# Performance work log

Hardware: AMD Instinct MI355X
Metric: run time of the kernel (lower is better)

The kernel has to match this reference:

```python
import jax, jax.numpy as jnp
import numpy as np

N, NQ, M, DQ, DK, DV, H = 4, 512, 512, 256, 256, 256, 256


def setup_inputs() -> dict:
    key = jax.random.key(0)
    ks = jax.random.split(key, 6)
    scale_q = 1.0 / np.sqrt(DQ)
    scale_k = 1.0 / np.sqrt(DK)
    scale_v = 1.0 / np.sqrt(H)
    return {
        "query": jax.random.normal(ks[0], (N, NQ, DQ), jnp.float32),
        "key": jax.random.normal(ks[1], (N, M, DK), jnp.float32),
        "value": jax.random.normal(ks[2], (N, M, DV), jnp.float32),
        "W_q": jax.random.normal(ks[3], (DQ, H), jnp.float32) * scale_q,
        "W_k": jax.random.normal(ks[4], (DK, H), jnp.float32) * scale_k,
        "W_v": jax.random.normal(ks[5], (H,), jnp.float32) * scale_v,
    }


def reference(query, key, value, W_q, W_k, W_v):
    # project: (N, n, H) and (N, m, H)
    q = jnp.einsum("bnd,dh->bnh", query, W_q)
    k = jnp.einsum("bmd,dh->bmh", key, W_k)
    # broadcast add -> (N, n, m, H), tanh, project H->1 -> scores (N, n, m)
    scores = jnp.einsum("bnmh,h->bnm", jnp.tanh(q[:, :, None, :] + k[:, None, :, :]), W_v)
    attn = jax.nn.softmax(scores, axis=-1)  # (N, n, m)
    return jnp.einsum("bnm,bmv->bnv", attn, value)
```

## Files before the change

kernel.cpp:

```cpp
#include <hip/hip_runtime.h>
#include <hip/hip_bf16.h>

#define NB 4
#define NQL 512
#define ML 512
#define DDIM 256
#define HDIM 256

static constexpr float TWO_LOG2E = 2.8853900817779268f;
static constexpr float LOG2E     = 1.4426950408889634f;

__global__ __launch_bounds__(256) void proj_kernel(
    const float* __restrict__ q_src, const float* __restrict__ k_src,
    const float* __restrict__ Wq,    const float* __restrict__ Wk,
    float* __restrict__ EqT,         float* __restrict__ EkT)
{
    const int z = blockIdx.z;
    const int b = z & 3;
    const int which = z >> 2;
    const float* __restrict__ src  = which ? k_src : q_src;
    const float* __restrict__ W    = which ? Wk    : Wq;
    float* __restrict__       outT = which ? EkT   : EqT;

    const int l0 = blockIdx.x * 32;
    const int h0 = blockIdx.y * 64;
    const int t  = threadIdx.x;
    const int tx = t & 15;
    const int ty = t >> 4;

    __shared__ float sX[32][36];
    __shared__ float sW[32][68];

    float acc[2][4];
    #pragma unroll
    for (int i = 0; i < 2; i++)
        #pragma unroll
        for (int j = 0; j < 4; j++) acc[i][j] = 0.f;

    const int llA = t >> 3, dgA = t & 7;
    const int ddB = t >> 3, hgB = t & 7;

    for (int d0 = 0; d0 < DDIM; d0 += 32) {
        float4 xv = *(const float4*)&src[(size_t)(b * NQL + l0 + llA) * DDIM + d0 + dgA * 4];
        const float* wrow = &W[(size_t)(d0 + ddB) * HDIM + h0 + hgB * 8];
        float4 wa = ((const float4*)wrow)[0];
        float4 wb = ((const float4*)wrow)[1];
        __syncthreads();
        sX[dgA * 4 + 0][llA] = xv.x;
        sX[dgA * 4 + 1][llA] = xv.y;
        sX[dgA * 4 + 2][llA] = xv.z;
        sX[dgA * 4 + 3][llA] = xv.w;
        *(float4*)&sW[ddB][hgB * 8]     = wa;
        *(float4*)&sW[ddB][hgB * 8 + 4] = wb;
        __syncthreads();
        #pragma unroll
        for (int dd = 0; dd < 32; dd++) {
            float4 w4 = *(const float4*)&sW[dd][tx * 4];
            float2 x2 = *(const float2*)&sX[dd][ty * 2];
            acc[0][0] = fmaf(x2.x, w4.x, acc[0][0]);
            acc[0][1] = fmaf(x2.x, w4.y, acc[0][1]);
            acc[0][2] = fmaf(x2.x, w4.z, acc[0][2]);
            acc[0][3] = fmaf(x2.x, w4.w, acc[0][3]);
            acc[1][0] = fmaf(x2.y, w4.x, acc[1][0]);
            acc[1][1] = fmaf(x2.y, w4.y, acc[1][1]);
            acc[1][2] = fmaf(x2.y, w4.z, acc[1][2]);
            acc[1][3] = fmaf(x2.y, w4.w, acc[1][3]);
        }
    }

    #pragma unroll
    for (int j = 0; j < 4; j++) {
        float2 o;
        o.x = __builtin_amdgcn_exp2f(acc[0][j] * TWO_LOG2E);
        o.y = __builtin_amdgcn_exp2f(acc[1][j] * TWO_LOG2E);
        *(float2*)&outT[(size_t)(b * HDIM + h0 + tx * 4 + j) * NQL + l0 + ty * 2] = o;
    }
}

__global__ __launch_bounds__(256) void scores_kernel(
    const float* __restrict__ EqT, const float* __restrict__ EkT,
    const float* __restrict__ Wv, float* __restrict__ S)
{
    const int b  = blockIdx.z;
    const int m0 = blockIdx.x * 32;
    const int n0 = blockIdx.y * 32;
    const int t  = threadIdx.x;
    const int tx = t & 15;
    const int ty = t >> 4;

    __shared__ float sQ[32][36];
    __shared__ float sK[32][36];
    __shared__ float sWV[32];

    float acc00 = 0.f, acc01 = 0.f, acc10 = 0.f, acc11 = 0.f;
    float swv = 0.f;

    const int hhA = t >> 3, cgA = t & 7;

    for (int h0 = 0; h0 < HDIM; h0 += 32) {
        float4 qv = *(const float4*)&EqT[(size_t)(b * HDIM + h0 + hhA) * NQL + n0 + cgA * 4];
        float4 kv = *(const float4*)&EkT[(size_t)(b * HDIM + h0 + hhA) * ML  + m0 + cgA * 4];
        float wv_ld = (t < 32) ? Wv[h0 + t] : 0.f;
        __syncthreads();
        *(float4*)&sQ[hhA][cgA * 4] = qv;
        *(float4*)&sK[hhA][cgA * 4] = kv;
        if (t < 32) sWV[t] = wv_ld;
        __syncthreads();
        #pragma unroll 8
        for (int hh = 0; hh < 32; hh++) {
            float2 q2 = *(const float2*)&sQ[hh][ty * 2];
            float2 k2 = *(const float2*)&sK[hh][tx * 2];
            float wv = sWV[hh];
            swv += wv;
            const float nw2 = -2.0f * wv;
            float a00 = fmaf(q2.x, k2.x, 1.0f);
            float a01 = fmaf(q2.x, k2.y, 1.0f);
            float a10 = fmaf(q2.y, k2.x, 1.0f);
            float a11 = fmaf(q2.y, k2.y, 1.0f);
            float r0 = __builtin_amdgcn_rcpf(a00 * a01);
            float r1 = __builtin_amdgcn_rcpf(a10 * a11);
            acc00 = fmaf(nw2, r0 * a01, acc00);
            acc01 = fmaf(nw2, r0 * a00, acc01);
            acc10 = fmaf(nw2, r1 * a11, acc10);
            acc11 = fmaf(nw2, r1 * a10, acc11);
        }
    }

    float2 o0 = {swv + acc00, swv + acc01};
    float2 o1 = {swv + acc10, swv + acc11};
    *(float2*)&S[(size_t)(b * NQL + n0 + ty * 2 + 0) * ML + m0 + tx * 2] = o0;
    *(float2*)&S[(size_t)(b * NQL + n0 + ty * 2 + 1) * ML + m0 + tx * 2] = o1;
}

__global__ __launch_bounds__(256) void softmax_kernel(float* __restrict__ S)
{
    const int row = blockIdx.x;
    float* p = &S[(size_t)row * ML];
    const int t = threadIdx.x;
    const int lane = t & 63, wid = t >> 6;

    float a = p[t];
    float c = p[t + 256];
    float mx = fmaxf(a, c);
    #pragma unroll
    for (int off = 32; off > 0; off >>= 1)
        mx = fmaxf(mx, __shfl_down(mx, off, 64));

    __shared__ float red[8];
    if (lane == 0) red[wid] = mx;
    __syncthreads();
    mx = fmaxf(fmaxf(red[0], red[1]), fmaxf(red[2], red[3]));

    float e0 = __builtin_amdgcn_exp2f((a - mx) * LOG2E);
    float e1 = __builtin_amdgcn_exp2f((c - mx) * LOG2E);
    float s = e0 + e1;
    #pragma unroll
    for (int off = 32; off > 0; off >>= 1)
        s += __shfl_down(s, off, 64);
    if (lane == 0) red[4 + wid] = s;
    __syncthreads();
    const float tot = red[4] + red[5] + red[6] + red[7];
    const float inv = 1.0f / tot;
    p[t]       = e0 * inv;
    p[t + 256] = e1 * inv;
}

__global__ __launch_bounds__(256) void av_kernel(
    const float* __restrict__ A, const float* __restrict__ V,
    float* __restrict__ O)
{
    const int b  = blockIdx.z;
    const int v0 = blockIdx.x * 64;
    const int n0 = blockIdx.y * 16;
    const int t  = threadIdx.x;
    const int tx = t & 15;
    const int ty = t >> 4;

    __shared__ float sA[32][20];
    __shared__ float sV[32][68];

    float4 acc = {0.f, 0.f, 0.f, 0.f};

    const int nnA = t >> 4, mgA = t & 15;
    const int mmB = t >> 3, vgB = t & 7;

    for (int m0 = 0; m0 < ML; m0 += 32) {
        float2 av = *(const float2*)&A[(size_t)(b * NQL + n0 + nnA) * ML + m0 + mgA * 2];
        const float* vrow = &V[(size_t)(b * ML + m0 + mmB) * DDIM + v0 + vgB * 8];
        float4 va = ((const float4*)vrow)[0];
        float4 vb = ((const float4*)vrow)[1];
        __syncthreads();
        sA[mgA * 2 + 0][nnA] = av.x;
        sA[mgA * 2 + 1][nnA] = av.y;
        *(float4*)&sV[mmB][vgB * 8]     = va;
        *(float4*)&sV[mmB][vgB * 8 + 4] = vb;
        __syncthreads();
        #pragma unroll
        for (int mm = 0; mm < 32; mm++) {
            float a = sA[mm][ty];
            float4 v4 = *(const float4*)&sV[mm][tx * 4];
            acc.x = fmaf(a, v4.x, acc.x);
            acc.y = fmaf(a, v4.y, acc.y);
            acc.z = fmaf(a, v4.z, acc.z);
            acc.w = fmaf(a, v4.w, acc.w);
        }
    }

    *(float4*)&O[(size_t)(b * NQL + n0 + ty) * DDIM + v0 + tx * 4] = acc;
}

extern "C" void kernel_launch(void* const* d_in, const int* in_sizes, int n_in,
                              void* d_out, int out_size, void* d_ws, size_t ws_size,
                              hipStream_t stream)
{
    const float* query = (const float*)d_in[0];
    const float* key   = (const float*)d_in[1];
    const float* value = (const float*)d_in[2];
    const float* Wq    = (const float*)d_in[3];
    const float* Wk    = (const float*)d_in[4];
    const float* Wv    = (const float*)d_in[5];
    float* out = (float*)d_out;

    float* EqT = (float*)d_ws;
    float* EkT = EqT + (size_t)NB * HDIM * NQL;
    float* S   = EkT + (size_t)NB * HDIM * ML;

    dim3 gProj(NQL / 32, HDIM / 64, NB * 2);
    proj_kernel<<<gProj, 256, 0, stream>>>(query, key, Wq, Wk, EqT, EkT);

    dim3 gSc(ML / 32, NQL / 32, NB);
    scores_kernel<<<gSc, 256, 0, stream>>>(EqT, EkT, Wv, S);

    softmax_kernel<<<dim3(NB * NQL), 256, 0, stream>>>(S);

    dim3 gAv(DDIM / 64, NQL / 16, NB);
    av_kernel<<<gAv, 256, 0, stream>>>(S, value, out);
}
```

Before: 133.7 us.

## Fuse softmax into scores and AV kernels via partial row sums

Drops the standalone softmax kernel. The scores kernel now writes unnormalized exponentials of the scores and per-tile partial row sums. The AV kernel sums these partials and scales its output by the reciprocal. This removes a kernel launch and a full read/write pass over the score matrix. It relies on scores being bounded, since no row max is subtracted, so it carries overflow risk for large weights.

```diff
diff --git a/kernel.cpp b/kernel.cpp
--- a/kernel.cpp
+++ b/kernel.cpp
@@ -79,10 +79,12 @@
 
 __global__ __launch_bounds__(256) void scores_kernel(
     const float* __restrict__ EqT, const float* __restrict__ EkT,
-    const float* __restrict__ Wv, float* __restrict__ S)
+    const float* __restrict__ Wv, float* __restrict__ P,
+    float* __restrict__ Spart)
 {
     const int b  = blockIdx.z;
-    const int m0 = blockIdx.x * 32;
+    const int mt = blockIdx.x;
+    const int m0 = mt * 32;
     const int n0 = blockIdx.y * 32;
     const int t  = threadIdx.x;
     const int tx = t & 15;
@@ -126,48 +128,30 @@
         }
     }
 
-    float2 o0 = {swv + acc00, swv + acc01};
-    float2 o1 = {swv + acc10, swv + acc11};
-    *(float2*)&S[(size_t)(b * NQL + n0 + ty * 2 + 0) * ML + m0 + tx * 2] = o0;
-    *(float2*)&S[(size_t)(b * NQL + n0 + ty * 2 + 1) * ML + m0 + tx * 2] = o1;
-}
-
-__global__ __launch_bounds__(256) void softmax_kernel(float* __restrict__ S)
-{
-    const int row = blockIdx.x;
-    float* p = &S[(size_t)row * ML];
-    const int t = threadIdx.x;
-    const int lane = t & 63, wid = t >> 6;
-
-    float a = p[t];
-    float c = p[t + 256];
-    float mx = fmaxf(a, c);
+    float2 o0, o1;
+    o0.x = __builtin_amdgcn_exp2f((swv + acc00) * LOG2E);
+    o0.y = __builtin_amdgcn_exp2f((swv + acc01) * LOG2E);
+    o1.x = __builtin_amdgcn_exp2f((swv + acc10) * LOG2E);
+    o1.y = __builtin_amdgcn_exp2f((swv + acc11) * LOG2E);
+    *(float2*)&P[(size_t)(b * NQL + n0 + ty * 2 + 0) * ML + m0 + tx * 2] = o0;
+    *(float2*)&P[(size_t)(b * NQL + n0 + ty * 2 + 1) * ML + m0 + tx * 2] = o1;
+
+    float rs0 = o0.x + o0.y;
+    float rs1 = o1.x + o1.y;
     #pragma unroll
-    for (int off = 32; off > 0; off >>= 1)
-        mx = fmaxf(mx, __shfl_down(mx, off, 64));
-
-    __shared__ float red[8];
-    if (lane == 0) red[wid] = mx;
-    __syncthreads();
-    mx = fmaxf(fmaxf(red[0], red[1]), fmaxf(red[2], red[3]));
-
-    float e0 = __builtin_amdgcn_exp2f((a - mx) * LOG2E);
-    float e1 = __builtin_amdgcn_exp2f((c - mx) * LOG2E);
-    float s = e0 + e1;
-    #pragma unroll
-    for (int off = 32; off > 0; off >>= 1)
-        s += __shfl_down(s, off, 64);
-    if (lane == 0) red[4 + wid] = s;
-    __syncthreads();
-    const float tot = red[4] + red[5] + red[6] + red[7];
-    const float inv = 1.0f / tot;
-    p[t]       = e0 * inv;
-    p[t + 256] = e1 * inv;
+    for (int off = 1; off < 16; off <<= 1) {
+        rs0 += __shfl_xor(rs0, off);
+        rs1 += __shfl_xor(rs1, off);
+    }
+    if (tx == 0) {
+        Spart[(size_t)(mt * NB + b) * NQL + n0 + ty * 2 + 0] = rs0;
+        Spart[(size_t)(mt * NB + b) * NQL + n0 + ty * 2 + 1] = rs1;
+    }
 }
 
 __global__ __launch_bounds__(256) void av_kernel(
-    const float* __restrict__ A, const float* __restrict__ V,
-    float* __restrict__ O)
+    const float* __restrict__ A, const float* __restrict__ Spart,
+    const float* __restrict__ V, float* __restrict__ O)
 {
     const int b  = blockIdx.z;
     const int v0 = blockIdx.x * 64;
@@ -178,6 +162,15 @@
 
     __shared__ float sA[32][20];
     __shared__ float sV[32][68];
+    __shared__ float sInv[16];
+
+    if (t < 16) {
+        float s = 0.f;
+        #pragma unroll
+        for (int mt = 0; mt < 16; ++mt)
+            s += Spart[(size_t)(mt * NB + b) * NQL + n0 + t];
+        sInv[t] = 1.0f / s;
+    }
 
     float4 acc = {0.f, 0.f, 0.f, 0.f};
 
@@ -206,7 +199,13 @@
         }
     }
 
-    *(float4*)&O[(size_t)(b * NQL + n0 + ty) * DDIM + v0 + tx * 4] = acc;
+    const float inv = sInv[ty];
+    float4 o;
+    o.x = acc.x * inv;
+    o.y = acc.y * inv;
+    o.z = acc.z * inv;
+    o.w = acc.w * inv;
+    *(float4*)&O[(size_t)(b * NQL + n0 + ty) * DDIM + v0 + tx * 4] = o;
 }
 
 extern "C" void kernel_launch(void* const* d_in, const int* in_sizes, int n_in,
@@ -221,18 +220,17 @@
     const float* Wv    = (const float*)d_in[5];
     float* out = (float*)d_out;
 
-    float* EqT = (float*)d_ws;
-    float* EkT = EqT + (size_t)NB * HDIM * NQL;
-    float* S   = EkT + (size_t)NB * HDIM * ML;
+    float* EqT   = (float*)d_ws;
+    float* EkT   = EqT + (size_t)NB * HDIM * NQL;
+    float* P     = EkT + (size_t)NB * HDIM * ML;
+    float* Spart = P + (size_t)NB * NQL * ML;
 
     dim3 gProj(NQL / 32, HDIM / 64, NB * 2);
     proj_kernel<<<gProj, 256, 0, stream>>>(query, key, Wq, Wk, EqT, EkT);
 
     dim3 gSc(ML / 32, NQL / 32, NB);
-    scores_kernel<<<gSc, 256, 0, stream>>>(EqT, EkT, Wv, S);
-
-    softmax_kernel<<<dim3(NB * NQL), 256, 0, stream>>>(S);
+    scores_kernel<<<gSc, 256, 0, stream>>>(EqT, EkT, Wv, P, Spart);
 
     dim3 gAv(DDIM / 64, NQL / 16, NB);
-    av_kernel<<<gAv, 256, 0, stream>>>(S, value, out);
-}
+    av_kernel<<<gAv, 256, 0, stream>>>(P, Spart, value, out);
+}
```

Result: no change. 133.6 us (-0.1%).
